# Optimization experiments

Measured on AMD Instinct MI355X. Metric: run time of the kernel, lower is better.

## Reference

```python
import jax, jax.numpy as jnp
import numpy as np

B, S, D, H = 2, 2048, 1024, 16
DK = D // H


def setup_inputs() -> dict:
    key = jax.random.key(0)
    ks = jax.random.split(key, 11)
    inp = {
        'query': jax.random.normal(ks[0], (B, S, D), jnp.float32),
        'key':   jax.random.normal(ks[1], (B, S, D), jnp.float32),
        'value': jax.random.normal(ks[2], (B, S, D), jnp.float32),
        # causal mask, broadcast over heads like mask.unsqueeze(1)
        'mask': jnp.broadcast_to(jnp.tril(jnp.ones((S, S), jnp.int32)), (B, S, S)),
    }
    s = 1.0 / np.sqrt(D)
    for i, nm in enumerate(['q', 'k', 'v', 'o']):
        inp[f'W{nm}'] = jax.random.normal(ks[3 + i], (D, D), jnp.float32) * s
        inp[f'b{nm}'] = jnp.zeros((D,), jnp.float32)
    return inp


def reference(query, key, value, mask, Wq, bq, Wk, bk, Wv, bv, Wo, bo):
    def proj(x, W, b):
        # [B,S,D] -> [B,H,S,DK]
        y = x @ W.T + b
        return y.reshape(B, S, H, DK).transpose(0, 2, 1, 3)

    q = proj(query, Wq, bq)
    k = proj(key, Wk, bk)
    v = proj(value, Wv, bv)

    scores = jnp.einsum('bhsd,bhtd->bhst', q, k) / np.sqrt(DK)
    scores = jnp.where(mask[:, None, :, :] == 0, -1e9, scores)
    p = jax.nn.softmax(scores, axis=-1)  # dropout in eval mode = identity
    x = jnp.einsum('bhst,bhtd->bhsd', p, v)
    x = x.transpose(0, 2, 1, 3).reshape(B, S, D)
    return x @ Wo.T + bo
```

## Files before the change

kernel.cpp:

```cpp
#include <hip/hip_runtime.h>
#include <stdint.h>

#define BB 2
#define SS 2048
#define DD 1024
#define HH 16
#define DKK 64
#define EE 4194304
#define WEE 1048576
#define QSCALE 0.1803368801f

typedef __attribute__((ext_vector_type(8))) short bf16x8;
typedef __attribute__((ext_vector_type(4))) float f32x4;
typedef __attribute__((ext_vector_type(4))) unsigned short u16x4;

__device__ __forceinline__ unsigned short f2bf(float f) {
    union { float f; unsigned int i; } c; c.f = f;
    unsigned int u = c.i;
    return (unsigned short)((u + 0x7FFFu + ((u >> 16) & 1u)) >> 16);
}
__device__ __forceinline__ float bf2f(unsigned short u) {
    union { float f; unsigned int i; } c; c.i = ((unsigned int)u) << 16; return c.f;
}
__device__ __forceinline__ float load1f(const void* p, int idx, int isbf) {
    return isbf ? bf2f(((const unsigned short*)p)[idx]) : ((const float*)p)[idx];
}

#define GLDS16(gp, lp)                                                              \
    __builtin_amdgcn_global_load_lds(                                               \
        (const __attribute__((address_space(1))) void*)(gp),                        \
        (__attribute__((address_space(3))) void*)(lp), 16, 0, 0)

__global__ void detect_dtype_k(const unsigned short* __restrict__ q,
                               int* __restrict__ flag) {
    const int lane = threadIdx.x;
    unsigned short u = q[lane * 2];
    int ex = (u >> 7) & 0xFF;
    bool bad = (ex != 0) && (ex < 110 || ex > 137);
    unsigned long long m = __ballot(bad);
    if (lane == 0) *flag = (__popcll(m) >= 8) ? 0 : 1;
}

__global__ __launch_bounds__(256)
void convert_k(const float* __restrict__ q, const float* __restrict__ k,
               const float* __restrict__ v,
               const float* __restrict__ wq, const float* __restrict__ wk,
               const float* __restrict__ wv, const float* __restrict__ wo,
               unsigned short* __restrict__ Xc, unsigned short* __restrict__ Wc,
               const int* __restrict__ flagp)
{
    if (*flagp) return;
    const size_t e = ((size_t)blockIdx.x * 256 + threadIdx.x) * 8;
    const float* src; unsigned short* dst; size_t off;
    if (e < (size_t)3 * EE) {
        const int t = (int)(e / EE);
        src = (t == 0) ? q : (t == 1) ? k : v;
        off = e - (size_t)t * EE;
        dst = Xc + (size_t)t * EE;
    } else {
        const size_t we = e - (size_t)3 * EE;
        const int t = (int)(we >> 20);
        src = (t == 0) ? wq : (t == 1) ? wk : (t == 2) ? wv : wo;
        off = we & (WEE - 1);
        dst = Wc + (size_t)t * WEE;
    }
    const float4 a = *(const float4*)(src + off);
    const float4 b = *(const float4*)(src + off + 4);
    bf16x8 o;
    o[0] = (short)f2bf(a.x); o[1] = (short)f2bf(a.y);
    o[2] = (short)f2bf(a.z); o[3] = (short)f2bf(a.w);
    o[4] = (short)f2bf(b.x); o[5] = (short)f2bf(b.y);
    o[6] = (short)f2bf(b.z); o[7] = (short)f2bf(b.w);
    *(bf16x8*)(dst + off) = o;
}

__global__ __launch_bounds__(256)
void gemm_qkv(const void* __restrict__ Xq, const void* __restrict__ Xk,
              const void* __restrict__ Xv,
              const void* __restrict__ Wqp, const void* __restrict__ Wkp,
              const void* __restrict__ Wvp,
              const void* __restrict__ bqp, const void* __restrict__ bkp,
              const void* __restrict__ bvp,
              const unsigned short* __restrict__ Xc,
              const unsigned short* __restrict__ Wc,
              unsigned short* __restrict__ qb, unsigned short* __restrict__ kb,
              unsigned short* __restrict__ vtb, const int* __restrict__ flagp)
{
    const int isbf = *flagp;
    const int z = blockIdx.z;
    const unsigned short* Xg = isbf
        ? (const unsigned short*)((z == 0) ? Xq : (z == 1) ? Xk : Xv)
        : Xc + (size_t)z * EE;
    const unsigned short* Wg = isbf
        ? (const unsigned short*)((z == 0) ? Wqp : (z == 1) ? Wkp : Wvp)
        : Wc + (size_t)z * WEE;
    const void* bias = (z == 0) ? bqp : (z == 1) ? bkp : bvp;

    __shared__ __align__(16) unsigned short As[128 * 32];
    __shared__ __align__(16) unsigned short Bs[128 * 32];

    const int tid  = threadIdx.x;
    const int lane = tid & 63, w = tid >> 6;
    const int l15  = lane & 15, quad = lane >> 4;
    const int wr = (w >> 1) * 64, wc = (w & 1) * 64;
    const int r0 = blockIdx.x * 128, c0 = blockIdx.y * 128;
    const int srow = tid >> 2, scol = (tid & 3) << 3;

    f32x4 acc[4][4] = {};

    for (int k0 = 0; k0 < DD; k0 += 32) {
        __syncthreads();
        GLDS16(Xg + (size_t)(r0 + srow) * DD + k0 + scol,       As + tid * 8);
        GLDS16(Xg + (size_t)(r0 + 64 + srow) * DD + k0 + scol,  As + 2048 + tid * 8);
        GLDS16(Wg + (size_t)(c0 + srow) * DD + k0 + scol,       Bs + tid * 8);
        GLDS16(Wg + (size_t)(c0 + 64 + srow) * DD + k0 + scol,  Bs + 2048 + tid * 8);
        __syncthreads();

        bf16x8 af[4], bfr[4];
#pragma unroll
        for (int mi = 0; mi < 4; ++mi)
            af[mi] = *(const bf16x8*)(As + (wr + mi * 16 + l15) * 32 + quad * 8);
#pragma unroll
        for (int ni = 0; ni < 4; ++ni)
            bfr[ni] = *(const bf16x8*)(Bs + (wc + ni * 16 + l15) * 32 + quad * 8);
#pragma unroll
        for (int mi = 0; mi < 4; ++mi)
#pragma unroll
            for (int ni = 0; ni < 4; ++ni)
                acc[mi][ni] = __builtin_amdgcn_mfma_f32_16x16x32_bf16(
                    af[mi], bfr[ni], acc[mi][ni], 0, 0, 0);
    }

#pragma unroll
    for (int mi = 0; mi < 4; ++mi) {
#pragma unroll
        for (int ni = 0; ni < 4; ++ni) {
            const int col = c0 + wc + ni * 16 + l15;
            const float bv = load1f(bias, col, isbf);
            const int h = col >> 6, dk = col & 63;
            const int m0 = r0 + wr + mi * 16 + quad * 4;
            const int bb = m0 >> 11, s0 = m0 & (SS - 1);
            const int bh = bb * HH + h;
            if (z == 0) {
#pragma unroll
                for (int r = 0; r < 4; ++r)
                    qb[((size_t)bh * SS + s0 + r) * DKK + dk] =
                        f2bf((acc[mi][ni][r] + bv) * QSCALE);
            } else if (z == 1) {
#pragma unroll
                for (int r = 0; r < 4; ++r) {
                    const int t = s0 + r;
                    kb[((((size_t)bh * 128 + (t >> 4)) * 8 + (dk >> 3)) * 16 +
                        (t & 15)) * 8 + (dk & 7)] = f2bf(acc[mi][ni][r] + bv);
                }
            } else {
                u16x4 pv;
#pragma unroll
                for (int r = 0; r < 4; ++r) pv[r] = f2bf(acc[mi][ni][r] + bv);
                const int t = s0;
                *(u16x4*)&vtb[((((size_t)bh * 64 + (t >> 5)) * 4 + (dk >> 4)) * 64 +
                               ((t >> 3) & 3) * 16 + (dk & 15)) * 8 + (t & 7)] = pv;
            }
        }
    }
}

template <bool MASKED>
__device__ __forceinline__ void attn_tile(
    const int t0, const int q0, const int l15, const int quad,
    const unsigned short* __restrict__ Kb, const unsigned short* __restrict__ Vb,
    const bf16x8 (&qf)[2], f32x4 (&Oa)[4], float (&ls)[4],
    unsigned short* __restrict__ Pw)
{
    bf16x8 kf[4][2];
#pragma unroll
    for (int ni = 0; ni < 4; ++ni)
#pragma unroll
        for (int ks = 0; ks < 2; ++ks)
            kf[ni][ks] = *(const bf16x8*)(Kb +
                ((size_t)(((t0 >> 4) + ni) * 8 + ks * 4 + quad) * 16 + l15) * 8);

    f32x4 sc[4] = {};
#pragma unroll
    for (int ks = 0; ks < 2; ++ks)
#pragma unroll
        for (int ni = 0; ni < 4; ++ni)
            sc[ni] = __builtin_amdgcn_mfma_f32_16x16x32_bf16(
                qf[ks], kf[ni][ks], sc[ni], 0, 0, 0);

    bf16x8 vf[4][2];
#pragma unroll
    for (int nd = 0; nd < 4; ++nd)
#pragma unroll
        for (int ks = 0; ks < 2; ++ks)
            vf[nd][ks] = *(const bf16x8*)(Vb +
                ((size_t)(((t0 >> 5) + ks) * 4 + nd) * 64 + quad * 16 + l15) * 8);

#pragma unroll
    for (int ni = 0; ni < 4; ++ni)
#pragma unroll
        for (int r = 0; r < 4; ++r) {
            float s = sc[ni][r];
            if (MASKED && (t0 + ni * 16 + l15 > q0 + quad * 4 + r))
                s = -__builtin_inff();
            const float p = exp2f(s);
            const unsigned int pu = __float_as_uint(p);
            ls[r] += __uint_as_float(pu & 0xFFFF0000u);
            Pw[(quad * 4 + r) * 72 + ni * 16 + l15] = (unsigned short)(pu >> 16);
        }

    bf16x8 pf[2];
#pragma unroll
    for (int ks = 0; ks < 2; ++ks)
        pf[ks] = *(const bf16x8*)(Pw + l15 * 72 + ks * 32 + quad * 8);
#pragma unroll
    for (int ks = 0; ks < 2; ++ks)
#pragma unroll
        for (int nd = 0; nd < 4; ++nd)
            Oa[nd] = __builtin_amdgcn_mfma_f32_16x16x32_bf16(
                pf[ks], vf[nd][ks], Oa[nd], 0, 0, 0);
}

__global__ __launch_bounds__(256)
void attn_mfma(const unsigned short* __restrict__ Qg,
               const unsigned short* __restrict__ Kf,
               const unsigned short* __restrict__ Vf,
               unsigned short* __restrict__ Og)
{
    __shared__ __align__(16) unsigned short Ps[4][16 * 72];
    const int tid  = threadIdx.x;
    const int lane = tid & 63, w = tid >> 6;
    const int l15 = lane & 15, quad = lane >> 4;
    const int bh = blockIdx.x;
    const int qt = (gridDim.y - 1 - blockIdx.y) * 4 + w;
    const int q0 = qt * 16;
    unsigned short* Pw = &Ps[w][0];

    const unsigned short* Qb = Qg + (size_t)bh * SS * DKK;
    const unsigned short* Kb = Kf + (size_t)bh * SS * DKK;
    const unsigned short* Vb = Vf + (size_t)bh * SS * DKK;

    bf16x8 qf[2];
#pragma unroll
    for (int ks = 0; ks < 2; ++ks)
        qf[ks] = *(const bf16x8*)(Qb + (size_t)(q0 + l15) * DKK + ks * 32 + quad * 8);

    f32x4 Oa[4] = {};
    float ls[4] = {};
    const int nfull = q0 >> 6;

    for (int tt = 0; tt < nfull; ++tt)
        attn_tile<false>(tt * 64, q0, l15, quad, Kb, Vb, qf, Oa, ls, Pw);
    attn_tile<true>(nfull * 64, q0, l15, quad, Kb, Vb, qf, Oa, ls, Pw);

    const int bb = bh >> 4, h = bh & (HH - 1);
#pragma unroll
    for (int r = 0; r < 4; ++r) {
        float l = ls[r];
        l += __shfl_xor(l, 1);
        l += __shfl_xor(l, 2);
        l += __shfl_xor(l, 4);
        l += __shfl_xor(l, 8);
        const float inv = 1.0f / l;
        const int s = q0 + quad * 4 + r;
#pragma unroll
        for (int nd = 0; nd < 4; ++nd)
            Og[((size_t)bb * SS + s) * DD + h * 64 + nd * 16 + l15] =
                f2bf(Oa[nd][r] * inv);
    }
}

__global__ __launch_bounds__(256)
void gemm_out(const unsigned short* __restrict__ Xa, const void* __restrict__ W,
              const unsigned short* __restrict__ Wcs,
              const void* __restrict__ bias, void* __restrict__ Y,
              const int* __restrict__ flagp)
{
    const int isbf = *flagp;
    const unsigned short* Wg = isbf ? (const unsigned short*)W : Wcs;

    __shared__ __align__(16) unsigned short As[128 * 32];
    __shared__ __align__(16) unsigned short Bs[128 * 32];

    const int tid  = threadIdx.x;
    const int lane = tid & 63, w = tid >> 6;
    const int l15  = lane & 15, quad = lane >> 4;
    const int wr = (w >> 1) * 64, wc = (w & 1) * 64;
    const int r0 = blockIdx.x * 128, c0 = blockIdx.y * 128;
    const int srow = tid >> 2, scol = (tid & 3) << 3;

    f32x4 acc[4][4] = {};

    for (int k0 = 0; k0 < DD; k0 += 32) {
        __syncthreads();
        GLDS16(Xa + (size_t)(r0 + srow) * DD + k0 + scol,       As + tid * 8);
        GLDS16(Xa + (size_t)(r0 + 64 + srow) * DD + k0 + scol,  As + 2048 + tid * 8);
        GLDS16(Wg + (size_t)(c0 + srow) * DD + k0 + scol,       Bs + tid * 8);
        GLDS16(Wg + (size_t)(c0 + 64 + srow) * DD + k0 + scol,  Bs + 2048 + tid * 8);
        __syncthreads();

        bf16x8 af[4], bfr[4];
#pragma unroll
        for (int mi = 0; mi < 4; ++mi)
            af[mi] = *(const bf16x8*)(As + (wr + mi * 16 + l15) * 32 + quad * 8);
#pragma unroll
        for (int ni = 0; ni < 4; ++ni)
            bfr[ni] = *(const bf16x8*)(Bs + (wc + ni * 16 + l15) * 32 + quad * 8);
#pragma unroll
        for (int mi = 0; mi < 4; ++mi)
#pragma unroll
            for (int ni = 0; ni < 4; ++ni)
                acc[mi][ni] = __builtin_amdgcn_mfma_f32_16x16x32_bf16(
                    af[mi], bfr[ni], acc[mi][ni], 0, 0, 0);
    }

#pragma unroll
    for (int mi = 0; mi < 4; ++mi) {
#pragma unroll
        for (int ni = 0; ni < 4; ++ni) {
            const int col = c0 + wc + ni * 16 + l15;
            const float bv = load1f(bias, col, isbf);
            const int m0 = r0 + wr + mi * 16 + quad * 4;
#pragma unroll
            for (int r = 0; r < 4; ++r) {
                const float val = acc[mi][ni][r] + bv;
                if (isbf) ((unsigned short*)Y)[(size_t)(m0 + r) * DD + col] = f2bf(val);
                else      ((float*)Y)[(size_t)(m0 + r) * DD + col] = val;
            }
        }
    }
}

extern "C" void kernel_launch(void* const* d_in, const int* in_sizes, int n_in,
                              void* d_out, int out_size, void* d_ws, size_t ws_size,
                              hipStream_t stream)
{
    const void* query = d_in[0];
    const void* key   = d_in[1];
    const void* value = d_in[2];
    const void* Wq = d_in[4];  const void* bq = d_in[5];
    const void* Wk = d_in[6];  const void* bk = d_in[7];
    const void* Wv = d_in[8];  const void* bv = d_in[9];
    const void* Wo = d_in[10]; const void* bo = d_in[11];

    int* flag = (int*)d_ws;
    unsigned short* base = (unsigned short*)((char*)d_ws + 256);
    const size_t E = EE;
    unsigned short* qb  = base;
    unsigned short* kb  = base + E;
    unsigned short* vtb = base + 2 * E;
    unsigned short* Wc  = base + 3 * E;
    unsigned short* Xc  = base + 4 * E;
    unsigned short* ab  = Xc;

    detect_dtype_k<<<1, 64, 0, stream>>>((const unsigned short*)query, flag);
    convert_k<<<8192, 256, 0, stream>>>((const float*)query, (const float*)key,
                                        (const float*)value, (const float*)Wq,
                                        (const float*)Wk, (const float*)Wv,
                                        (const float*)Wo, Xc, Wc, flag);
    gemm_qkv<<<dim3(32, 8, 3), 256, 0, stream>>>(query, key, value, Wq, Wk, Wv,
                                                 bq, bk, bv, Xc, Wc,
                                                 qb, kb, vtb, flag);
    attn_mfma<<<dim3(32, 32), 256, 0, stream>>>(qb, kb, vtb, ab);
    gemm_out<<<dim3(32, 8), 256, 0, stream>>>(ab, Wo, Wc + 3 * (size_t)WEE, bo,
                                              d_out, flag);
}
```

Measured before the change: 257.2 us.

## Double-buffer LDS tiles in QKV and output GEMMs to overlap loads with MFMA

Both projection GEMMs now use two LDS buffers per operand. The next K-slice is issued via global-to-LDS loads before the MFMAs on the current slice run, with a single vmcnt wait and barrier per iteration instead of two syncthreads. This aims to hide global load latency behind compute. In exchange LDS use per block doubles, which may lower occupancy, and raw s_waitcnt/sched_barrier ordering is relied on for correctness.

New measurement: 247.0 us. 4.0% less time.

```diff
diff --git a/kernel.cpp b/kernel.cpp
--- a/kernel.cpp
+++ b/kernel.cpp
@@ -96,8 +96,8 @@
         : Wc + (size_t)z * WEE;
     const void* bias = (z == 0) ? bqp : (z == 1) ? bkp : bvp;
 
-    __shared__ __align__(16) unsigned short As[128 * 32];
-    __shared__ __align__(16) unsigned short Bs[128 * 32];
+    __shared__ __align__(16) unsigned short As[2][128 * 32];
+    __shared__ __align__(16) unsigned short Bs[2][128 * 32];
 
     const int tid  = threadIdx.x;
     const int lane = tid & 63, w = tid >> 6;
@@ -106,30 +106,56 @@
     const int r0 = blockIdx.x * 128, c0 = blockIdx.y * 128;
     const int srow = tid >> 2, scol = (tid & 3) << 3;
 
+    const unsigned short* xp0 = Xg + (size_t)(r0 + srow) * DD + scol;
+    const unsigned short* xp1 = Xg + (size_t)(r0 + 64 + srow) * DD + scol;
+    const unsigned short* wp0 = Wg + (size_t)(c0 + srow) * DD + scol;
+    const unsigned short* wp1 = Wg + (size_t)(c0 + 64 + srow) * DD + scol;
+
+#define STAGE_QKV(buf, kk)                                                     \
+    do {                                                                       \
+        GLDS16(xp0 + (kk), &As[buf][tid * 8]);                                 \
+        GLDS16(xp1 + (kk), &As[buf][2048 + tid * 8]);                          \
+        GLDS16(wp0 + (kk), &Bs[buf][tid * 8]);                                 \
+        GLDS16(wp1 + (kk), &Bs[buf][2048 + tid * 8]);                          \
+    } while (0)
+
+#define COMPUTE_QKV(buf)                                                       \
+    do {                                                                       \
+        bf16x8 af[4], bfr[4];                                                  \
+        _Pragma("unroll")                                                      \
+        for (int mi = 0; mi < 4; ++mi)                                         \
+            af[mi] = *(const bf16x8*)(&As[buf][(wr + mi * 16 + l15) * 32 +     \
+                                               quad * 8]);                     \
+        _Pragma("unroll")                                                      \
+        for (int ni = 0; ni < 4; ++ni)                                         \
+            bfr[ni] = *(const bf16x8*)(&Bs[buf][(wc + ni * 16 + l15) * 32 +    \
+                                                quad * 8]);                    \
+        _Pragma("unroll")                                                      \
+        for (int mi = 0; mi < 4; ++mi)                                         \
+            _Pragma("unroll")                                                  \
+            for (int ni = 0; ni < 4; ++ni)                                     \
+                acc[mi][ni] = __builtin_amdgcn_mfma_f32_16x16x32_bf16(         \
+                    af[mi], bfr[ni], acc[mi][ni], 0, 0, 0);                    \
+    } while (0)
+
     f32x4 acc[4][4] = {};
 
-    for (int k0 = 0; k0 < DD; k0 += 32) {
-        __syncthreads();
-        GLDS16(Xg + (size_t)(r0 + srow) * DD + k0 + scol,       As + tid * 8);
-        GLDS16(Xg + (size_t)(r0 + 64 + srow) * DD + k0 + scol,  As + 2048 + tid * 8);
-        GLDS16(Wg + (size_t)(c0 + srow) * DD + k0 + scol,       Bs + tid * 8);
-        GLDS16(Wg + (size_t)(c0 + 64 + srow) * DD + k0 + scol,  Bs + 2048 + tid * 8);
-        __syncthreads();
-
-        bf16x8 af[4], bfr[4];
-#pragma unroll
-        for (int mi = 0; mi < 4; ++mi)
-            af[mi] = *(const bf16x8*)(As + (wr + mi * 16 + l15) * 32 + quad * 8);
-#pragma unroll
-        for (int ni = 0; ni < 4; ++ni)
-            bfr[ni] = *(const bf16x8*)(Bs + (wc + ni * 16 + l15) * 32 + quad * 8);
-#pragma unroll
-        for (int mi = 0; mi < 4; ++mi)
-#pragma unroll
-            for (int ni = 0; ni < 4; ++ni)
-                acc[mi][ni] = __builtin_amdgcn_mfma_f32_16x16x32_bf16(
-                    af[mi], bfr[ni], acc[mi][ni], 0, 0, 0);
-    }
+    STAGE_QKV(0, 0);
+    asm volatile("s_waitcnt vmcnt(0)" ::: "memory");
+    __builtin_amdgcn_s_barrier();
+    __builtin_amdgcn_sched_barrier(0);
+
+    int cur = 0;
+    for (int k0 = 0; k0 < DD - 32; k0 += 32) {
+        STAGE_QKV(cur ^ 1, k0 + 32);
+        __builtin_amdgcn_sched_barrier(0);
+        COMPUTE_QKV(cur);
+        asm volatile("s_waitcnt vmcnt(0)" ::: "memory");
+        __builtin_amdgcn_s_barrier();
+        __builtin_amdgcn_sched_barrier(0);
+        cur ^= 1;
+    }
+    COMPUTE_QKV(cur);
 
 #pragma unroll
     for (int mi = 0; mi < 4; ++mi) {
@@ -163,6 +189,8 @@
             }
         }
     }
+#undef STAGE_QKV
+#undef COMPUTE_QKV
 }
 
 template <bool MASKED>
@@ -279,8 +307,8 @@
     const int isbf = *flagp;
     const unsigned short* Wg = isbf ? (const unsigned short*)W : Wcs;
 
-    __shared__ __align__(16) unsigned short As[128 * 32];
-    __shared__ __align__(16) unsigned short Bs[128 * 32];
+    __shared__ __align__(16) unsigned short As[2][128 * 32];
+    __shared__ __align__(16) unsigned short Bs[2][128 * 32];
 
     const int tid  = threadIdx.x;
     const int lane = tid & 63, w = tid >> 6;
@@ -289,30 +317,56 @@
     const int r0 = blockIdx.x * 128, c0 = blockIdx.y * 128;
     const int srow = tid >> 2, scol = (tid & 3) << 3;
 
+    const unsigned short* xp0 = Xa + (size_t)(r0 + srow) * DD + scol;
+    const unsigned short* xp1 = Xa + (size_t)(r0 + 64 + srow) * DD + scol;
+    const unsigned short* wp0 = Wg + (size_t)(c0 + srow) * DD + scol;
+    const unsigned short* wp1 = Wg + (size_t)(c0 + 64 + srow) * DD + scol;
+
+#define STAGE_OUT(buf, kk)                                                     \
+    do {                                                                       \
+        GLDS16(xp0 + (kk), &As[buf][tid * 8]);                                 \
+        GLDS16(xp1 + (kk), &As[buf][2048 + tid * 8]);                          \
+        GLDS16(wp0 + (kk), &Bs[buf][tid * 8]);                                 \
+        GLDS16(wp1 + (kk), &Bs[buf][2048 + tid * 8]);                          \
+    } while (0)
+
+#define COMPUTE_OUT(buf)                                                       \
+    do {                                                                       \
+        bf16x8 af[4], bfr[4];                                                  \
+        _Pragma("unroll")                                                      \
+        for (int mi = 0; mi < 4; ++mi)                                         \
+            af[mi] = *(const bf16x8*)(&As[buf][(wr + mi * 16 + l15) * 32 +     \
+                                               quad * 8]);                     \
+        _Pragma("unroll")                                                      \
+        for (int ni = 0; ni < 4; ++ni)                                         \
+            bfr[ni] = *(const bf16x8*)(&Bs[buf][(wc + ni * 16 + l15) * 32 +    \
+                                                quad * 8]);                    \
+        _Pragma("unroll")                                                      \
+        for (int mi = 0; mi < 4; ++mi)                                         \
+            _Pragma("unroll")                                                  \
+            for (int ni = 0; ni < 4; ++ni)                                     \
+                acc[mi][ni] = __builtin_amdgcn_mfma_f32_16x16x32_bf16(         \
+                    af[mi], bfr[ni], acc[mi][ni], 0, 0, 0);                    \
+    } while (0)
+
     f32x4 acc[4][4] = {};
 
-    for (int k0 = 0; k0 < DD; k0 += 32) {
-        __syncthreads();
-        GLDS16(Xa + (size_t)(r0 + srow) * DD + k0 + scol,       As + tid * 8);
-        GLDS16(Xa + (size_t)(r0 + 64 + srow) * DD + k0 + scol,  As + 2048 + tid * 8);
-        GLDS16(Wg + (size_t)(c0 + srow) * DD + k0 + scol,       Bs + tid * 8);
-        GLDS16(Wg + (size_t)(c0 + 64 + srow) * DD + k0 + scol,  Bs + 2048 + tid * 8);
-        __syncthreads();
-
-        bf16x8 af[4], bfr[4];
-#pragma unroll
-        for (int mi = 0; mi < 4; ++mi)
-            af[mi] = *(const bf16x8*)(As + (wr + mi * 16 + l15) * 32 + quad * 8);
-#pragma unroll
-        for (int ni = 0; ni < 4; ++ni)
-            bfr[ni] = *(const bf16x8*)(Bs + (wc + ni * 16 + l15) * 32 + quad * 8);
-#pragma unroll
-        for (int mi = 0; mi < 4; ++mi)
-#pragma unroll
-            for (int ni = 0; ni < 4; ++ni)
-                acc[mi][ni] = __builtin_amdgcn_mfma_f32_16x16x32_bf16(
-                    af[mi], bfr[ni], acc[mi][ni], 0, 0, 0);
-    }
+    STAGE_OUT(0, 0);
+    asm volatile("s_waitcnt vmcnt(0)" ::: "memory");
+    __builtin_amdgcn_s_barrier();
+    __builtin_amdgcn_sched_barrier(0);
+
+    int cur = 0;
+    for (int k0 = 0; k0 < DD - 32; k0 += 32) {
+        STAGE_OUT(cur ^ 1, k0 + 32);
+        __builtin_amdgcn_sched_barrier(0);
+        COMPUTE_OUT(cur);
+        asm volatile("s_waitcnt vmcnt(0)" ::: "memory");
+        __builtin_amdgcn_s_barrier();
+        __builtin_amdgcn_sched_barrier(0);
+        cur ^= 1;
+    }
+    COMPUTE_OUT(cur);
 
 #pragma unroll
     for (int mi = 0; mi < 4; ++mi) {
@@ -329,6 +383,8 @@
             }
         }
     }
+#undef STAGE_OUT
+#undef COMPUTE_OUT
 }
 
 extern "C" void kernel_launch(void* const* d_in, const int* in_sizes, int n_in,
```
